# Performance work log

Hardware: AMD Instinct MI355X
Metric: run time of the kernel (lower is better)

## Reference

```python
import jax, jax.numpy as jnp
import numpy as np

B, T, C = 8, 2048, 1024
H, K = 16, 31  # num_heads, kernel_size; head_size = C // H = 64


def setup_inputs() -> dict:
    key = jax.random.key(0)
    ks = jax.random.split(key, 3)
    x = jax.random.normal(ks[0], (B, T, C), dtype=jnp.float32)
    Wk = jax.random.normal(ks[1], (C, 2 * C), dtype=jnp.float32) * 0.02
    bk = jnp.zeros((2 * C,), dtype=jnp.float32)
    Wck = jax.random.normal(ks[2], (C, K * H), dtype=jnp.float32) * 0.02
    bck = jnp.zeros((K * H,), dtype=jnp.float32)
    gamma = jnp.ones((C,), dtype=jnp.float32)
    beta = jnp.zeros((C,), dtype=jnp.float32)
    conv_bias = jnp.zeros((C,), dtype=jnp.float32)
    return {"x": x, "Wk": Wk, "bk": bk, "Wck": Wck, "bck": bck,
            "gamma": gamma, "beta": beta, "conv_bias": conv_bias}


def _layernorm(x, g, b, eps=1e-5):
    mu = jnp.mean(x, axis=-1, keepdims=True)
    var = jnp.mean(jnp.square(x - mu), axis=-1, keepdims=True)
    return (x - mu) * jax.lax.rsqrt(var + eps) * g + b


def reference(x, Wk, bk, Wck, bck, gamma, beta, conv_bias):
    b, t, c = x.shape
    hd = c // H  # head size
    h = _layernorm(x, gamma, beta)
    pre = h @ Wk + bk                      # [B,T,2C]
    a, gte = jnp.split(pre, 2, axis=-1)
    k = a * jax.nn.sigmoid(gte)            # GLU -> [B,T,C]
    w = (k @ Wck + bck).reshape(b, t, H, K)
    w = jax.nn.softmax(w, axis=-1)         # per-token per-head kernel
    pad = K // 2
    kp = jnp.pad(k, ((0, 0), (pad, pad), (0, 0))).reshape(b, t + 2 * pad, H, hd)
    # depthwise dynamic conv: sum over K shifted slices (no im2col blowup)
    out = sum(w[:, :, :, i:i + 1] * kp[:, i:i + t] for i in range(K))  # [B,T,H,hd]
    out = out.reshape(b, t, c) + conv_bias + x  # bias + residual
    return out
```

## Files before the change

kernel.cpp:

```cpp
#include <hip/hip_runtime.h>


typedef __bf16 bf16_t;
typedef __attribute__((ext_vector_type(8))) __bf16 bf16x8;
typedef __attribute__((ext_vector_type(4))) __bf16 bf16x4;
typedef __attribute__((ext_vector_type(4))) float f32x4;

__device__ __forceinline__ void gload_lds16(const void* g, void* l) {
  void* gg = const_cast<void*>(g);
  __builtin_amdgcn_global_load_lds(
      (__attribute__((address_space(1))) unsigned int*)gg,
      (__attribute__((address_space(3))) unsigned int*)l, 16, 0, 0);
}

__global__ __launch_bounds__(256) void prep_wk(const float* __restrict__ Wk,
                                               bf16_t* __restrict__ WT) {
  int c = blockIdx.x;
  int s = (c & 1) ? 1024 + (c >> 1) : (c >> 1);
  int k = threadIdx.x * 4;
  bf16x4 v;
#pragma unroll
  for (int j = 0; j < 4; ++j) v[j] = (bf16_t)Wk[(size_t)(k + j) * 2048 + s];
  *(bf16x4*)&WT[(size_t)c * 1024 + k] = v;
}

__global__ __launch_bounds__(256) void prep_wck(const float* __restrict__ Wck,
                                                bf16_t* __restrict__ WT) {
  int n = blockIdx.x;
  int k = threadIdx.x * 4;
  bf16x4 v;
#pragma unroll
  for (int j = 0; j < 4; ++j)
    v[j] = (n < 496) ? (bf16_t)Wck[(size_t)(k + j) * 496 + n] : (bf16_t)(0.f);
  *(bf16x4*)&WT[(size_t)n * 1024 + k] = v;
}

__global__ __launch_bounds__(256) void ln_kernel(const float* __restrict__ x,
                                                 const float* __restrict__ gamma,
                                                 const float* __restrict__ beta,
                                                 bf16_t* __restrict__ h) {
  int row = blockIdx.x;
  int tid = threadIdx.x;
  int lane = tid & 63, wid = tid >> 6;
  const float4* xr = (const float4*)(x + (size_t)row * 1024);
  float4 v = xr[tid];
  __shared__ float red[4];
  __shared__ float bc[2];
  float s = v.x + v.y + v.z + v.w;
#pragma unroll
  for (int off = 32; off > 0; off >>= 1) s += __shfl_down(s, off);
  if (lane == 0) red[wid] = s;
  __syncthreads();
  if (tid == 0) bc[0] = (red[0] + red[1] + red[2] + red[3]) * (1.f / 1024.f);
  __syncthreads();
  float mu = bc[0];
  float dx = v.x - mu, dy = v.y - mu, dz = v.z - mu, dw = v.w - mu;
  float s2 = dx * dx + dy * dy + dz * dz + dw * dw;
#pragma unroll
  for (int off = 32; off > 0; off >>= 1) s2 += __shfl_down(s2, off);
  if (lane == 0) red[wid] = s2;
  __syncthreads();
  if (tid == 0)
    bc[1] = rsqrtf((red[0] + red[1] + red[2] + red[3]) * (1.f / 1024.f) + 1e-5f);
  __syncthreads();
  float rs = bc[1];
  const float4* g4 = (const float4*)gamma;
  const float4* b4 = (const float4*)beta;
  float4 gv = g4[tid], bv = b4[tid];
  bf16x4 o;
  o[0] = (bf16_t)(dx * rs * gv.x + bv.x);
  o[1] = (bf16_t)(dy * rs * gv.y + bv.y);
  o[2] = (bf16_t)(dz * rs * gv.z + bv.z);
  o[3] = (bf16_t)(dw * rs * gv.w + bv.w);
  *(bf16x4*)&h[(size_t)row * 1024 + tid * 4] = o;
}

__global__ __launch_bounds__(512, 2) void gemm256_glu(const bf16_t* __restrict__ Ag,
                                                      const bf16_t* __restrict__ Bg,
                                                      const float* __restrict__ bias,
                                                      bf16_t* __restrict__ outp) {
  extern __shared__ char smem[];
  const int tid = threadIdx.x;
  const int lane = tid & 63;
  const int wid = tid >> 6;
  const int wr = wid >> 2;
  const int wc = wid & 3;

  int bid = blockIdx.x;
  int swz = (bid & 7) * 64 + (bid >> 3);
  int m0 = (swz >> 3) * 256;
  int n0 = (swz & 7) * 256;

  const int xr = (lane & 7) << 4;
  const int cs0 = (((lane >> 4) << 4) ^ xr);
  const int cs1 = cs0 ^ 64;
  const int aBase = wr * 16384 + (lane & 15) * 128;
  const int bBase = 65536 + (wc >> 1) * 16384 + (wc & 1) * 8192 + (lane & 15) * 128;

  const int sidx0 = tid, sidx1 = tid + 512;
  const int srow0 = sidx0 >> 3, srow1 = sidx1 >> 3;
  const int scol0 = ((((sidx0 & 7) << 4) ^ ((srow0 & 7) << 4)) >> 1);
  const int scol1 = ((((sidx1 & 7) << 4) ^ ((srow1 & 7) << 4)) >> 1);
  const int d0 = sidx0 * 16, d1 = sidx1 * 16;

  f32x4 acc[8][4] = {};
  bf16x8 bq[4][2];

#define STAGE_A(buf, h_, kt)                                                          \
  {                                                                                   \
    gload_lds16(Ag + (size_t)(m0 + (h_)*128 + srow0) * 1024 + (kt) + scol0,           \
                smem + (buf)*32768 + (h_)*16384 + d0);                                \
    gload_lds16(Ag + (size_t)(m0 + (h_)*128 + srow1) * 1024 + (kt) + scol1,           \
                smem + (buf)*32768 + (h_)*16384 + d1);                                \
  }
#define STAGE_B(buf, h_, kt)                                                          \
  {                                                                                   \
    gload_lds16(Bg + (size_t)(n0 + (h_)*128 + srow0) * 1024 + (kt) + scol0,           \
                smem + 65536 + (buf)*32768 + (h_)*16384 + d0);                        \
    gload_lds16(Bg + (size_t)(n0 + (h_)*128 + srow1) * 1024 + (kt) + scol1,           \
                smem + 65536 + (buf)*32768 + (h_)*16384 + d1);                        \
  }
#define LDA(buf, f, s) (*(const bf16x8*)(smem + (buf)*32768 + aBase + (f)*2048 + ((s) ? cs1 : cs0)))
#define LDB(buf, g, s) (*(const bf16x8*)(smem + bBase + (buf)*32768 + (g)*2048 + ((s) ? cs1 : cs0)))
#define MFMA_(a, b, c) __builtin_amdgcn_mfma_f32_16x16x32_bf16(a, b, c, 0, 0, 0)

#define PHASE(buf, f0, P0, STAGE_STMT, TAIL_VM)                                       \
  {                                                                                   \
    bf16x8 a00 = LDA(buf, f0, 0), a01 = LDA(buf, f0, 1);                              \
    bf16x8 a10 = LDA(buf, (f0) + 1, 0), a11 = LDA(buf, (f0) + 1, 1);                  \
    if (P0) {                                                                         \
      _Pragma("unroll") for (int g = 0; g < 4; ++g) {                                 \
        bq[g][0] = LDB(buf, g, 0);                                                    \
        bq[g][1] = LDB(buf, g, 1);                                                    \
      }                                                                               \
    }                                                                                 \
    STAGE_STMT;                                                                       \
    __builtin_amdgcn_s_barrier();                                                     \
    __builtin_amdgcn_s_setprio(1);                                                    \
    _Pragma("unroll") for (int g = 0; g < 4; ++g) {                                   \
      acc[f0][g] = MFMA_(a00, bq[g][0], acc[f0][g]);                                  \
      acc[f0][g] = MFMA_(a01, bq[g][1], acc[f0][g]);                                  \
      acc[(f0) + 1][g] = MFMA_(a10, bq[g][0], acc[(f0) + 1][g]);                      \
      acc[(f0) + 1][g] = MFMA_(a11, bq[g][1], acc[(f0) + 1][g]);                      \
    }                                                                                 \
    __builtin_amdgcn_s_setprio(0);                                                    \
    TAIL_VM;                                                                          \
    __builtin_amdgcn_s_barrier();                                                     \
  }

  STAGE_B(0, 0, 0); STAGE_B(0, 1, 0); STAGE_A(0, 0, 0); STAGE_A(0, 1, 0);
  STAGE_B(1, 0, 64); STAGE_B(1, 1, 64);
  asm volatile("s_waitcnt vmcnt(4)" ::: "memory");
  __builtin_amdgcn_s_barrier();

  for (int t = 0; t < 14; ++t) {
    const int buf = t & 1, nbuf = buf ^ 1;
    const int ktA = (t + 1) * 64, ktB = (t + 2) * 64;
    PHASE(buf, 0, 1, STAGE_A(nbuf, 0, ktA), ((void)0));
    PHASE(buf, 2, 0, STAGE_A(nbuf, 1, ktA), ((void)0));
    PHASE(buf, 4, 0, STAGE_B(buf, 0, ktB), ((void)0));
    PHASE(buf, 6, 0, STAGE_B(buf, 1, ktB),
          asm volatile("s_waitcnt vmcnt(4)" ::: "memory"));
  }
  PHASE(0, 0, 1, STAGE_A(1, 0, 960), ((void)0));
  PHASE(0, 2, 0, STAGE_A(1, 1, 960), ((void)0));
  PHASE(0, 4, 0, ((void)0), ((void)0));
  PHASE(0, 6, 0, ((void)0), asm volatile("s_waitcnt vmcnt(0)" ::: "memory"));
  PHASE(1, 0, 1, ((void)0), ((void)0));
  PHASE(1, 2, 0, ((void)0), ((void)0));
  PHASE(1, 4, 0, ((void)0), ((void)0));
  PHASE(1, 6, 0, ((void)0), ((void)0));

#pragma unroll
  for (int f = 0; f < 8; ++f) {
    int row = m0 + wr * 128 + f * 16 + ((lane >> 4) << 2);
#pragma unroll
    for (int g = 0; g < 4; ++g) {
      int col = n0 + wc * 64 + g * 16 + (lane & 15);
      int src = (col & 1) ? 1024 + (col >> 1) : (col >> 1);
      float bv = bias[src];
#pragma unroll
      for (int j = 0; j < 4; ++j) {
        float v = acc[f][g][j] + bv;
        float gt = __shfl_xor(v, 1);
        if (!(col & 1)) {
          float kv = v / (1.f + __expf(-gt));
          outp[(size_t)(row + j) * 1024 + (col >> 1)] = (bf16_t)kv;
        }
      }
    }
  }
#undef STAGE_A
#undef STAGE_B
#undef LDA
#undef LDB
#undef MFMA_
#undef PHASE
}

__global__ __launch_bounds__(256, 2) void gemm128_bias(const bf16_t* __restrict__ Ag,
                                                       const bf16_t* __restrict__ Bg,
                                                       const float* __restrict__ bias,
                                                       float* __restrict__ outp) {
  __shared__ bf16_t As[2][128 * 32];
  __shared__ bf16_t Bs[2][128 * 32];
  int tid = threadIdx.x;
  int lane = tid & 63;
  int wid = tid >> 6;
  int wr = wid >> 1, wc = wid & 1;
  int n0 = blockIdx.x * 128;
  int m0 = blockIdx.y * 128;

  f32x4 acc[4][4] = {};

#define STAGE(bufi, kt)                                                         \
  {                                                                             \
    _Pragma("unroll") for (int s_ = 0; s_ < 2; ++s_) {                          \
      int idx = (tid + s_ * 256) * 8;                                           \
      int row = idx >> 5;                                                       \
      int col = idx & 31;                                                       \
      gload_lds16(Ag + (size_t)(m0 + row) * 1024 + (kt) + col, &As[bufi][idx]); \
      gload_lds16(Bg + (size_t)(n0 + row) * 1024 + (kt) + col, &Bs[bufi][idx]); \
    }                                                                           \
  }

#define COMPUTE(bufi)                                                           \
  {                                                                             \
    int ko = (lane >> 4) * 8;                                                   \
    int rl = lane & 15;                                                         \
    bf16x8 af[4], bb[4];                                                        \
    _Pragma("unroll") for (int m_ = 0; m_ < 4; ++m_)                            \
        af[m_] = *(const bf16x8*)&As[bufi][(wr * 64 + m_ * 16 + rl) * 32 + ko]; \
    _Pragma("unroll") for (int n_ = 0; n_ < 4; ++n_)                            \
        bb[n_] = *(const bf16x8*)&Bs[bufi][(wc * 64 + n_ * 16 + rl) * 32 + ko]; \
    _Pragma("unroll") for (int m_ = 0; m_ < 4; ++m_)                            \
        _Pragma("unroll") for (int n_ = 0; n_ < 4; ++n_)                        \
            acc[m_][n_] = __builtin_amdgcn_mfma_f32_16x16x32_bf16(              \
                af[m_], bb[n_], acc[m_][n_], 0, 0, 0);                          \
  }

  STAGE(0, 0);
  __syncthreads();
  int buf = 0;
  for (int kt = 32; kt < 1024; kt += 32) {
    STAGE(buf ^ 1, kt);
    COMPUTE(buf);
    __syncthreads();
    buf ^= 1;
  }
  COMPUTE(buf);

#pragma unroll
  for (int m_ = 0; m_ < 4; ++m_) {
    int row = m0 + wr * 64 + m_ * 16 + ((lane >> 4) << 2);
#pragma unroll
    for (int n_ = 0; n_ < 4; ++n_) {
      int col = n0 + wc * 64 + n_ * 16 + (lane & 15);
      float bv = (col < 496) ? bias[col] : 0.f;
#pragma unroll
      for (int j = 0; j < 4; ++j)
        outp[(size_t)(row + j) * 512 + col] = acc[m_][n_][j] + bv;
    }
  }
#undef STAGE
#undef COMPUTE
}

__global__ __launch_bounds__(256) void conv_kernel(const bf16_t* __restrict__ Kin,
                                                   const float* __restrict__ logits,
                                                   const float* __restrict__ x,
                                                   const float* __restrict__ conv_bias,
                                                   float* __restrict__ out) {
  __shared__ bf16_t ks[94][64];
  __shared__ float wls[64][32];
  int tid = threadIdx.x;
  int t0 = blockIdx.x * 64;
  int hh = blockIdx.y;
  int b = blockIdx.z;

  for (int i = tid; i < 94 * 8; i += 256) {
    int r = i >> 3;
    int seg = (i & 7) * 8;
    int t = t0 - 15 + r;
    bf16x8 v = {};
    if (t >= 0 && t < 2048)
      v = *(const bf16x8*)&Kin[((size_t)b * 2048 + t) * 1024 + hh * 64 + seg];
    *(bf16x8*)&ks[r][seg] = v;
  }
  if (tid < 64) {
    int t = t0 + tid;
    const float* lp = logits + ((size_t)b * 2048 + t) * 512 + hh * 31;
    float l[31];
    float mx = -1e30f;
#pragma unroll
    for (int i = 0; i < 31; ++i) { l[i] = lp[i]; mx = fmaxf(mx, l[i]); }
    float ssum = 0.f;
#pragma unroll
    for (int i = 0; i < 31; ++i) { l[i] = __expf(l[i] - mx); ssum += l[i]; }
    float inv = 1.f / ssum;
#pragma unroll
    for (int i = 0; i < 31; ++i) wls[tid][i] = l[i] * inv;
  }
  __syncthreads();

  int lane = tid & 63;
  int tq = tid >> 6;
  float win[46];
#pragma unroll
  for (int j = 0; j < 46; ++j) win[j] = (float)ks[tq * 16 + j][lane];
  float cb = conv_bias[hh * 64 + lane];
#pragma unroll
  for (int j = 0; j < 16; ++j) {
    int trow = tq * 16 + j;
    float wv[31];
#pragma unroll
    for (int i4 = 0; i4 < 7; ++i4) {
      f32x4 w4 = *(const f32x4*)&wls[trow][i4 * 4];
      wv[i4 * 4 + 0] = w4[0]; wv[i4 * 4 + 1] = w4[1];
      wv[i4 * 4 + 2] = w4[2]; wv[i4 * 4 + 3] = w4[3];
    }
    wv[28] = wls[trow][28]; wv[29] = wls[trow][29]; wv[30] = wls[trow][30];
    float a = 0.f;
#pragma unroll
    for (int i = 0; i < 31; ++i) a += wv[i] * win[j + i];
    size_t off = ((size_t)b * 2048 + t0 + trow) * 1024 + hh * 64 + lane;
    out[off] = a + cb + x[off];
  }
}

extern "C" void kernel_launch(void* const* d_in, const int* in_sizes, int n_in,
                              void* d_out, int out_size, void* d_ws, size_t ws_size,
                              hipStream_t stream) {
  const float* x         = (const float*)d_in[0];
  const float* Wk        = (const float*)d_in[1];
  const float* bk        = (const float*)d_in[2];
  const float* Wck       = (const float*)d_in[3];
  const float* bck       = (const float*)d_in[4];
  const float* gamma     = (const float*)d_in[5];
  const float* beta      = (const float*)d_in[6];
  const float* conv_bias = (const float*)d_in[7];
  float* out = (float*)d_out;

  char* ws = (char*)d_ws;
  bf16_t* h      = (bf16_t*)(ws);
  bf16_t* kbuf   = (bf16_t*)(ws + (33554432));
  bf16_t* WT1    = (bf16_t*)(ws + (67108864));
  bf16_t* WT2    = (bf16_t*)(ws + (71303168));
  float*  logits = (float*)(ws + (72351744));

  hipFuncSetAttribute((const void*)gemm256_glu,
                      hipFuncAttributeMaxDynamicSharedMemorySize, 131072);

  prep_wk<<<2048, 256, 0, stream>>>(Wk, WT1);
  prep_wck<<<512, 256, 0, stream>>>(Wck, WT2);
  ln_kernel<<<16384, 256, 0, stream>>>(x, gamma, beta, h);
  gemm256_glu<<<512, 512, 131072, stream>>>(h, WT1, bk, kbuf);
  gemm128_bias<<<dim3(4, 128), 256, 0, stream>>>(kbuf, WT2, bck, logits);
  conv_kernel<<<dim3(32, 16, 8), 256, 0, stream>>>(kbuf, logits, x, conv_bias, out);
}
```

Before: 292.7 us.

## Tile weight transposes through LDS and software-pipeline LDS reads in GLU GEMM

```diff
diff --git a/kernel.cpp b/kernel.cpp
--- a/kernel.cpp
+++ b/kernel.cpp
@@ -15,24 +15,64 @@
 
 __global__ __launch_bounds__(256) void prep_wk(const float* __restrict__ Wk,
                                                bf16_t* __restrict__ WT) {
-  int c = blockIdx.x;
-  int s = (c & 1) ? 1024 + (c >> 1) : (c >> 1);
-  int k = threadIdx.x * 4;
-  bf16x4 v;
-#pragma unroll
-  for (int j = 0; j < 4; ++j) v[j] = (bf16_t)Wk[(size_t)(k + j) * 2048 + s];
-  *(bf16x4*)&WT[(size_t)c * 1024 + k] = v;
+  __shared__ bf16_t T[64][66];
+  int c0 = blockIdx.x * 64;
+  int k0 = blockIdx.y * 64;
+  int tid = threadIdx.x;
+#pragma unroll
+  for (int p = 0; p < 4; ++p) {
+    int idx = p * 256 + tid;
+    int r = idx >> 4;
+    int q = idx & 15;
+    int strip = q >> 3;
+    int col4 = (q & 7) * 4;
+    const float* src = Wk + (size_t)(k0 + r) * 2048 + strip * 1024 + (c0 >> 1) + col4;
+    float4 v = *(const float4*)src;
+#pragma unroll
+    for (int j = 0; j < 4; ++j) {
+      int cl = (col4 + j) * 2 + strip;
+      T[cl][r] = (bf16_t)((&v.x)[j]);
+    }
+  }
+  __syncthreads();
+  int c = tid >> 2;
+  int kk = (tid & 3) * 16;
+#pragma unroll
+  for (int u = 0; u < 2; ++u) {
+    bf16x8 o;
+#pragma unroll
+    for (int j = 0; j < 8; ++j) o[j] = T[c][kk + u * 8 + j];
+    *(bf16x8*)&WT[(size_t)(c0 + c) * 1024 + k0 + kk + u * 8] = o;
+  }
 }
 
 __global__ __launch_bounds__(256) void prep_wck(const float* __restrict__ Wck,
                                                 bf16_t* __restrict__ WT) {
-  int n = blockIdx.x;
-  int k = threadIdx.x * 4;
-  bf16x4 v;
-#pragma unroll
-  for (int j = 0; j < 4; ++j)
-    v[j] = (n < 496) ? (bf16_t)Wck[(size_t)(k + j) * 496 + n] : (bf16_t)(0.f);
-  *(bf16x4*)&WT[(size_t)n * 1024 + k] = v;
+  __shared__ bf16_t T[64][66];
+  int n0 = blockIdx.x * 64;
+  int k0 = blockIdx.y * 64;
+  int tid = threadIdx.x;
+#pragma unroll
+  for (int p = 0; p < 4; ++p) {
+    int idx = p * 256 + tid;
+    int r = idx >> 4;
+    int q = idx & 15;
+    int col = n0 + q * 4;
+    float4 v = {0.f, 0.f, 0.f, 0.f};
+    if (col < 496) v = *(const float4*)(Wck + (size_t)(k0 + r) * 496 + col);
+#pragma unroll
+    for (int j = 0; j < 4; ++j) T[q * 4 + j][r] = (bf16_t)((&v.x)[j]);
+  }
+  __syncthreads();
+  int c = tid >> 2;
+  int kk = (tid & 3) * 16;
+#pragma unroll
+  for (int u = 0; u < 2; ++u) {
+    bf16x8 o;
+#pragma unroll
+    for (int j = 0; j < 8; ++j) o[j] = T[c][kk + u * 8 + j];
+    *(bf16x8*)&WT[(size_t)(n0 + c) * 1024 + k0 + kk + u * 8] = o;
+  }
 }
 
 __global__ __launch_bounds__(256) void ln_kernel(const float* __restrict__ x,
@@ -104,7 +144,7 @@
   const int d0 = sidx0 * 16, d1 = sidx1 * 16;
 
   f32x4 acc[8][4] = {};
-  bf16x8 bq[4][2];
+  bf16x8 bq[4][2], pc[2][2], pn[2][2];
 
 #define STAGE_A(buf, h_, kt)                                                          \
   {                                                                                   \
@@ -123,53 +163,62 @@
 #define LDA(buf, f, s) (*(const bf16x8*)(smem + (buf)*32768 + aBase + (f)*2048 + ((s) ? cs1 : cs0)))
 #define LDB(buf, g, s) (*(const bf16x8*)(smem + bBase + (buf)*32768 + (g)*2048 + ((s) ? cs1 : cs0)))
 #define MFMA_(a, b, c) __builtin_amdgcn_mfma_f32_16x16x32_bf16(a, b, c, 0, 0, 0)
-
-#define PHASE(buf, f0, P0, STAGE_STMT, TAIL_VM)                                       \
+#define RD_PAIR(D, buf, f)                                                            \
+  { D[0][0] = LDA(buf, f, 0); D[0][1] = LDA(buf, f, 1);                               \
+    D[1][0] = LDA(buf, (f) + 1, 0); D[1][1] = LDA(buf, (f) + 1, 1); }
+#define RD_BQ(buf)                                                                    \
+  { _Pragma("unroll") for (int g = 0; g < 4; ++g) {                                   \
+      bq[g][0] = LDB(buf, g, 0); bq[g][1] = LDB(buf, g, 1); } }
+#define MM_PAIR(F0, P)                                                                \
+  { _Pragma("unroll") for (int g = 0; g < 4; ++g) {                                   \
+      acc[F0][g]       = MFMA_(P[0][0], bq[g][0], acc[F0][g]);                        \
+      acc[(F0) + 1][g] = MFMA_(P[1][0], bq[g][0], acc[(F0) + 1][g]);                  \
+      acc[F0][g]       = MFMA_(P[0][1], bq[g][1], acc[F0][g]);                        \
+      acc[(F0) + 1][g] = MFMA_(P[1][1], bq[g][1], acc[(F0) + 1][g]); } }
+#define LGKM0                                                                         \
+  asm volatile("s_waitcnt lgkmcnt(0)" ::: "memory");                                  \
+  __builtin_amdgcn_sched_barrier(0)
+#define BAR __builtin_amdgcn_s_barrier()
+#define PRIO1 __builtin_amdgcn_s_setprio(1)
+#define PRIO0 __builtin_amdgcn_s_setprio(0)
+
+#define TILE(BUF, NBUF, T)                                                            \
   {                                                                                   \
-    bf16x8 a00 = LDA(buf, f0, 0), a01 = LDA(buf, f0, 1);                              \
-    bf16x8 a10 = LDA(buf, (f0) + 1, 0), a11 = LDA(buf, (f0) + 1, 1);                  \
-    if (P0) {                                                                         \
-      _Pragma("unroll") for (int g = 0; g < 4; ++g) {                                 \
-        bq[g][0] = LDB(buf, g, 0);                                                    \
-        bq[g][1] = LDB(buf, g, 1);                                                    \
-      }                                                                               \
-    }                                                                                 \
-    STAGE_STMT;                                                                       \
-    __builtin_amdgcn_s_barrier();                                                     \
-    __builtin_amdgcn_s_setprio(1);                                                    \
-    _Pragma("unroll") for (int g = 0; g < 4; ++g) {                                   \
-      acc[f0][g] = MFMA_(a00, bq[g][0], acc[f0][g]);                                  \
-      acc[f0][g] = MFMA_(a01, bq[g][1], acc[f0][g]);                                  \
-      acc[(f0) + 1][g] = MFMA_(a10, bq[g][0], acc[(f0) + 1][g]);                      \
-      acc[(f0) + 1][g] = MFMA_(a11, bq[g][1], acc[(f0) + 1][g]);                      \
-    }                                                                                 \
-    __builtin_amdgcn_s_setprio(0);                                                    \
-    TAIL_VM;                                                                          \
-    __builtin_amdgcn_s_barrier();                                                     \
+                                                                              \
+    BAR;                                                                              \
+    if ((T) < 15) { STAGE_A(NBUF, 0, ((T) + 1) * 64); STAGE_A(NBUF, 1, ((T) + 1) * 64); } \
+    LGKM0; PRIO1; MM_PAIR(0, pc); PRIO0;                                              \
+    RD_PAIR(pn, BUF, 2);                                                              \
+                                                                              \
+    BAR;                                                                              \
+    LGKM0; PRIO1; MM_PAIR(2, pn); PRIO0;                                              \
+    RD_PAIR(pc, BUF, 4);                                                              \
+                                                                              \
+    BAR;                                                                              \
+    if ((T) < 14) STAGE_B(BUF, 0, ((T) + 2) * 64);                                    \
+    LGKM0; PRIO1; MM_PAIR(4, pc); PRIO0;                                              \
+    RD_PAIR(pn, BUF, 6);                                                              \
+                                                                              \
+    if ((T) < 14)       { asm volatile("s_waitcnt vmcnt(2)" ::: "memory"); }          \
+    else if ((T) == 14) { asm volatile("s_waitcnt vmcnt(0)" ::: "memory"); }          \
+    BAR;                                                                              \
+    if ((T) < 14) STAGE_B(BUF, 1, ((T) + 2) * 64);                                    \
+    LGKM0; PRIO1; MM_PAIR(6, pn); PRIO0;                                              \
+    if ((T) < 15) { RD_BQ(NBUF); RD_PAIR(pc, NBUF, 0); }                              \
   }
 
   STAGE_B(0, 0, 0); STAGE_B(0, 1, 0); STAGE_A(0, 0, 0); STAGE_A(0, 1, 0);
   STAGE_B(1, 0, 64); STAGE_B(1, 1, 64);
   asm volatile("s_waitcnt vmcnt(4)" ::: "memory");
-  __builtin_amdgcn_s_barrier();
-
-  for (int t = 0; t < 14; ++t) {
-    const int buf = t & 1, nbuf = buf ^ 1;
-    const int ktA = (t + 1) * 64, ktB = (t + 2) * 64;
-    PHASE(buf, 0, 1, STAGE_A(nbuf, 0, ktA), ((void)0));
-    PHASE(buf, 2, 0, STAGE_A(nbuf, 1, ktA), ((void)0));
-    PHASE(buf, 4, 0, STAGE_B(buf, 0, ktB), ((void)0));
-    PHASE(buf, 6, 0, STAGE_B(buf, 1, ktB),
-          asm volatile("s_waitcnt vmcnt(4)" ::: "memory"));
-  }
-  PHASE(0, 0, 1, STAGE_A(1, 0, 960), ((void)0));
-  PHASE(0, 2, 0, STAGE_A(1, 1, 960), ((void)0));
-  PHASE(0, 4, 0, ((void)0), ((void)0));
-  PHASE(0, 6, 0, ((void)0), asm volatile("s_waitcnt vmcnt(0)" ::: "memory"));
-  PHASE(1, 0, 1, ((void)0), ((void)0));
-  PHASE(1, 2, 0, ((void)0), ((void)0));
-  PHASE(1, 4, 0, ((void)0), ((void)0));
-  PHASE(1, 6, 0, ((void)0), ((void)0));
+  BAR;
+  RD_BQ(0); RD_PAIR(pc, 0, 0);
+
+  for (int t = 0; t < 14; t += 2) {
+    TILE(0, 1, t);
+    TILE(1, 0, t + 1);
+  }
+  TILE(0, 1, 14);
+  TILE(1, 0, 15);
 
 #pragma unroll
   for (int f = 0; f < 8; ++f) {
@@ -195,7 +244,14 @@
 #undef LDA
 #undef LDB
 #undef MFMA_
-#undef PHASE
+#undef RD_PAIR
+#undef RD_BQ
+#undef MM_PAIR
+#undef LGKM0
+#undef BAR
+#undef PRIO1
+#undef PRIO0
+#undef TILE
 }
 
 __global__ __launch_bounds__(256, 2) void gemm128_bias(const bf16_t* __restrict__ Ag,
@@ -351,8 +407,8 @@
   hipFuncSetAttribute((const void*)gemm256_glu,
                       hipFuncAttributeMaxDynamicSharedMemorySize, 131072);
 
-  prep_wk<<<2048, 256, 0, stream>>>(Wk, WT1);
-  prep_wck<<<512, 256, 0, stream>>>(Wck, WT2);
+  prep_wk<<<dim3(32, 16), 256, 0, stream>>>(Wk, WT1);
+  prep_wck<<<dim3(8, 16), 256, 0, stream>>>(Wck, WT2);
   ln_kernel<<<16384, 256, 0, stream>>>(x, gamma, beta, h);
   gemm256_glu<<<512, 512, 131072, stream>>>(h, WT1, bk, kbuf);
   gemm128_bias<<<dim3(4, 128), 256, 0, stream>>>(kbuf, WT2, bck, logits);
```

After: 290.6 us. Within noise of the previous version (-0.7%).
